# Performance work log

Hardware: AMD Instinct MI355X
Metric: run time of the kernel (lower is better)

Reference implementation:

```python
import jax, jax.numpy as jnp
import numpy as np
import math

SR = 24000
NH = 100      # num_harmonics
NF = 5        # num_formants
HID = 128
TWO_PI = 2.0 * math.pi


def conv1d(x, w, b, groups=1):
    # x: [B,C,T], w: [O, C//groups, K] (torch OIH layout), 'same' padding
    pad = (w.shape[-1] - 1) // 2
    y = jax.lax.conv_general_dilated(
        x, w, window_strides=(1,), padding=[(pad, pad)],
        dimension_numbers=('NCH', 'OIH', 'NCH'), feature_group_count=groups)
    return y + b[None, :, None]


def lrelu(x):
    return jnp.where(x >= 0, x, 0.1 * x)


def interp_linear(x, L):
    # torch F.interpolate(mode='linear', align_corners=False): x [B,C,T] -> [B,C,L]
    B, C, T = x.shape
    pos = (jnp.arange(L, dtype=x.dtype) + 0.5) * (T / L) - 0.5
    pos = jnp.clip(pos, 0.0, float(T - 1))
    lo = jnp.floor(pos).astype(jnp.int32)
    hi = jnp.minimum(lo + 1, T - 1)
    w = pos - lo.astype(x.dtype)
    return x[:, :, lo] * (1.0 - w) + x[:, :, hi] * w


def setup_inputs():
    key = jax.random.key(0)
    ks = jax.random.split(key, 30)
    ki = iter(range(30))
    def p(shape, s=0.05):
        return s * jax.random.normal(ks[next(ki)], shape, jnp.float32)
    B, T, L = 4, 500, 120000
    inp = {}
    # f0 in [80,120) Hz so actual_harmonics == num_harmonics (static shapes, see notes)
    inp['f0'] = 80.0 + 40.0 * jax.random.uniform(ks[next(ki)], (B, T), jnp.float32)
    inp['condition'] = jax.random.normal(ks[next(ki)], (B, HID, T), jnp.float32)
    # harmonic_amplitude_net params
    inp['ha_w1'] = p((HID, 1, 3));   inp['ha_b1'] = p((HID,))
    inp['ha_w2'] = p((256, HID, 1)); inp['ha_b2'] = p((256,))
    inp['ha_w3'] = p((256, 1, 3));   inp['ha_b3'] = p((256,))
    inp['ha_w4'] = p((256, 256, 1)); inp['ha_b4'] = p((256,))
    inp['ha_w5'] = p((NH, 256, 1));  inp['ha_b5'] = p((NH,))
    # formant predictor params
    inp['fm_w1'] = p((256, HID, 3));    inp['fm_b1'] = p((256,))
    inp['fm_w2'] = p((256, 256, 3));    inp['fm_b2'] = p((256,))
    inp['fm_w3'] = p((2 * NF, 256, 1)); inp['fm_b3'] = p((2 * NF,))
    # voice quality predictor params
    inp['vq_w1'] = p((128, HID, 3)); inp['vq_b1'] = p((128,))
    inp['vq_w2'] = p((64, 128, 3));  inp['vq_b2'] = p((64,))
    inp['vq_w3'] = p((3, 64, 1));    inp['vq_b3'] = p((3,))
    inp['audio_length'] = L
    return inp


def reference(f0, condition,
              ha_w1, ha_b1, ha_w2, ha_b2, ha_w3, ha_b3, ha_w4, ha_b4, ha_w5, ha_b5,
              fm_w1, fm_b1, fm_w2, fm_b2, fm_w3, fm_b3,
              vq_w1, vq_b1, vq_w2, vq_b2, vq_w3, vq_b3,
              audio_length):
    B, T = f0.shape
    L = audio_length
    # ---- harmonic_amplitude_net: (dw3 -> pw1 -> lrelu) x2 -> pw1 -> softplus ----
    a = lrelu(conv1d(conv1d(condition, ha_w1, ha_b1, groups=HID), ha_w2, ha_b2))
    a = lrelu(conv1d(conv1d(a, ha_w3, ha_b3, groups=256), ha_w4, ha_b4))
    harmonic_amplitudes = jax.nn.softplus(conv1d(a, ha_w5, ha_b5))  # [B,NH,T]
    # ---- FormantNetwork ----
    fp = conv1d(lrelu(conv1d(lrelu(conv1d(condition, fm_w1, fm_b1)), fm_w2, fm_b2)), fm_w3, fm_b3)
    ff = 200.0 + 3300.0 * jax.nn.sigmoid(fp[:, :NF])        # [B,NF,T]
    fbw = 50.0 + 150.0 * jax.nn.softplus(fp[:, NF:])        # [B,NF,T]
    hidx = jnp.arange(1, NH + 1, dtype=f0.dtype)
    hfreq = hidx[None, :, None] * f0[:, None, :]            # [B,NH,T]
    num = fbw ** 2                                          # [B,NF,T]
    den = (hfreq[:, None] - ff[:, :, None]) ** 2 + num[:, :, None]  # [B,NF,NH,T]
    res = num[:, :, None] / jnp.maximum(den, 1e-5)
    gain = jnp.prod(0.8 + 0.2 * res, axis=1)                # [B,NH,T]
    shaped = harmonic_amplitudes * gain
    # ---- VoiceQualityNetwork ----
    q = jax.nn.sigmoid(conv1d(lrelu(conv1d(lrelu(conv1d(condition, vq_w1, vq_b1)), vq_w2, vq_b2)), vq_w3, vq_b3))
    q_up = interp_linear(q, L)                              # [B,3,L]
    jitter = q_up[:, 0] * 0.05
    shimmer = q_up[:, 1] * 0.15
    breath = q_up[:, 2] * 0.3
    # ---- phase integration + harmonic bank ----
    f0_up = interp_linear(f0[:, None, :], L)[:, 0]          # [B,L]
    phase = jnp.cumsum(TWO_PI * f0_up / SR, axis=1)
    nk1, nk2, nk3 = jax.random.split(jax.random.key(42), 3)
    jphase = phase + jitter * jax.random.normal(nk1, phase.shape, phase.dtype)
    mask = (hidx[None, :, None] * f0_up[:, None, :] < SR / 2).astype(f0.dtype)  # [B,NH,L]
    amps_up = interp_linear(shaped, L)                      # [B,NH,L]
    sig = jnp.sum(amps_up * jnp.sin(jphase[:, None, :] * hidx[None, :, None]) * mask, axis=1)
    # ---- voice qualities: shimmer envelope + breath noise ----
    shim_env = 1.0 + jax.random.normal(nk2, sig.shape, sig.dtype) * shimmer
    out = sig * shim_env + jax.random.normal(nk3, sig.shape, sig.dtype) * breath
    return out
```

## Files before the change

kernel.cpp:

```cpp
#include <hip/hip_runtime.h>
#include <stdint.h>

#define B_ 4
#define T_ 500
#define L_ 120000
#define NH_ 100
#define N1_ 7500
#define N2_ 469
#define N2P_ 7504
#define N3_ 30
#define N3P_ 480
#define N4_ 2
#define N4P_ 32

#define ACT_NONE 0
#define ACT_LRELU 1
#define ACT_SOFTPLUS 2
#define ACT_SIGMOID 3

#define CH3 32
#define XN 4352
#define WN 1536
#define BUFA (XN + WN)

typedef const __attribute__((address_space(1))) void* gp1_t;
typedef __attribute__((address_space(3))) void* lp3_t;

__host__ __device__ __forceinline__ uint32_t tf_rotl(uint32_t v, int d) {
  return (v << d) | (v >> (32 - d));
}
__host__ __device__ __forceinline__ void tf_block(uint32_t k0, uint32_t k1,
                                                  uint32_t& x0, uint32_t& x1) {
  uint32_t k2 = k0 ^ k1 ^ 0x1BD11BDAu;
  x0 += k0; x1 += k1;
#define TF_R(d) x0 += x1; x1 = tf_rotl(x1, (d)); x1 ^= x0;
  TF_R(13) TF_R(15) TF_R(26) TF_R(6)   x0 += k1; x1 += k2 + 1u;
  TF_R(17) TF_R(29) TF_R(16) TF_R(24)  x0 += k2; x1 += k0 + 2u;
  TF_R(13) TF_R(15) TF_R(26) TF_R(6)   x0 += k0; x1 += k1 + 3u;
  TF_R(17) TF_R(29) TF_R(16) TF_R(24)  x0 += k1; x1 += k2 + 4u;
  TF_R(13) TF_R(15) TF_R(26) TF_R(6)   x0 += k2; x1 += k0 + 5u;
#undef TF_R
}

__device__ __forceinline__ float erfinv_xla(float x) {
  float w = -log1pf(-(x * x));
  float p;
  if (w < 5.0f) {
    w = w - 2.5f;
    p = 2.81022636e-08f;
    p = fmaf(p, w, 3.43273939e-07f);
    p = fmaf(p, w, -3.5233877e-06f);
    p = fmaf(p, w, -4.39150654e-06f);
    p = fmaf(p, w, 0.00021858087f);
    p = fmaf(p, w, -0.00125372503f);
    p = fmaf(p, w, -0.00417768164f);
    p = fmaf(p, w, 0.246640727f);
    p = fmaf(p, w, 1.50140941f);
  } else {
    w = sqrtf(w) - 3.0f;
    p = -0.000200214257f;
    p = fmaf(p, w, 0.000100950558f);
    p = fmaf(p, w, 0.00134934322f);
    p = fmaf(p, w, -0.00367342844f);
    p = fmaf(p, w, 0.00573950773f);
    p = fmaf(p, w, -0.0076224613f);
    p = fmaf(p, w, 0.00943887047f);
    p = fmaf(p, w, 1.00167406f);
    p = fmaf(p, w, 2.83297682f);
  }
  return p * x;
}

__device__ __forceinline__ float jax_normal(uint32_t k0, uint32_t k1, uint32_t e) {
  uint32_t x0 = 0u, x1 = e;
  tf_block(k0, k1, x0, x1);
  uint32_t bits = x0 ^ x1;
  float u = __uint_as_float((bits >> 9) | 0x3f800000u) - 1.0f;
  float v = __fadd_rn(__fmul_rn(u, 2.0f), -0x1.fffffep-1f);
  v = fmaxf(v, -0x1.fffffep-1f);
  return __fmul_rn((float)1.4142135623730951, erfinv_xla(v));
}

__device__ __forceinline__ float sin_acc(float xf) {
  double x = (double)xf;
  double kd = rint(x * 6.3661977236758138e-01);
  double r = fma(-kd, 1.5707963267948966e+00, x);
  r = fma(-kd, 6.1232339957367660e-17, r);
  float rf = (float)r;
  float y = rf * rf;
  float ps = fmaf(y, 2.7557319e-06f, -1.9841270e-04f);
  ps = fmaf(y, ps, 8.3333335e-03f);
  ps = fmaf(y, ps, -0.16666667f);
  float s = fmaf(rf * y, ps, rf);
  float pc = fmaf(y, -2.7557319e-07f, 2.4801587e-05f);
  pc = fmaf(y, pc, -1.3888889e-03f);
  pc = fmaf(y, pc, 4.1666668e-02f);
  pc = fmaf(y, pc, -0.5f);
  float c = fmaf(y, pc, 1.0f);
  int q = ((int)kd) & 3;
  float rs = (q & 1) ? c : s;
  return (q & 2) ? -rs : rs;
}

__device__ __forceinline__ float apply_act(float v, int act) {
  switch (act) {
    case ACT_LRELU:    return v >= 0.0f ? v : 0.1f * v;
    case ACT_SOFTPLUS: return fmaxf(v, 0.0f) + log1pf(expf(-fabsf(v)));
    case ACT_SIGMOID:  return 1.0f / (1.0f + expf(-v));
  }
  return v;
}


__device__ __forceinline__ void conv3_async(
    const float* __restrict__ x, const float* __restrict__ w,
    const float* __restrict__ bias, float* __restrict__ y,
    const float* __restrict__ zbuf,
    int Cin, int Cout, int o0, int act, int b, int t0, float* smem) {
  int tid = threadIdx.x;
  int lane = tid & 63, og = tid >> 6;
  int tl = 2 * lane;
  int t = t0 + tl;
  int obase = o0 + og * 4;
  float acc[4][2];
#pragma unroll
  for (int i = 0; i < 4; ++i) {
    float bv = (obase + i < Cout) ? bias[obase + i] : 0.0f;
    acc[i][0] = bv; acc[i][1] = bv;
  }
  const int nch = Cin / CH3;
  auto issue = [&](int c, float* buf) {
    int cb = c * CH3;
#pragma unroll
    for (int k = 0; k < 17; ++k) {
      int idx = tid + 256 * k;
      const float* src = zbuf;
      if (idx < CH3 * 130) {
        int cc = idx / 130, j = idx - cc * 130;
        int tt = t0 - 1 + j;
        if (tt >= 0 && tt < T_) src = x + ((size_t)b * Cin + cb + cc) * T_ + tt;
      }
      __builtin_amdgcn_global_load_lds((gp1_t)src, (lp3_t)(buf + idx), 4, 0, 0);
    }
#pragma unroll
    for (int k = 0; k < 6; ++k) {
      int p = tid + 256 * k;
      int cc = p / 48, r = p - cc * 48;
      int oo = r / 3, kk = r - oo * 3;
      const float* src = (o0 + oo < Cout)
          ? w + ((size_t)(o0 + oo) * Cin + cb + cc) * 3 + kk : zbuf;
      __builtin_amdgcn_global_load_lds((gp1_t)src, (lp3_t)(buf + XN + p), 4, 0, 0);
    }
  };
  issue(0, smem);
  for (int c = 0; c < nch; ++c) {
    const float* cur = smem + (c & 1) * BUFA;
    if (c + 1 < nch) {
      issue(c + 1, smem + ((c + 1) & 1) * BUFA);
      asm volatile("s_waitcnt vmcnt(23)" ::: "memory");
    } else {
      asm volatile("s_waitcnt vmcnt(0)" ::: "memory");
    }
    __builtin_amdgcn_s_barrier();
    __builtin_amdgcn_sched_barrier(0);
    const float* sxf = cur;
    const float* swf = cur + XN;
    for (int cc = 0; cc < CH3; ++cc) {
      const float* row = sxf + cc * 130 + tl;
      float2 xa = *(const float2*)row;
      float2 xb = *(const float2*)(row + 2);
      const float4* wq = (const float4*)(swf + cc * 48 + og * 12);
      float4 W0 = wq[0], W1 = wq[1], W2 = wq[2];
      float wl[12] = {W0.x, W0.y, W0.z, W0.w, W1.x, W1.y, W1.z, W1.w,
                      W2.x, W2.y, W2.z, W2.w};
#pragma unroll
      for (int i = 0; i < 4; ++i) {
        float w0 = wl[3 * i], w1 = wl[3 * i + 1], w2 = wl[3 * i + 2];
        acc[i][0] = fmaf(xa.x, w0, acc[i][0]);
        acc[i][0] = fmaf(xa.y, w1, acc[i][0]);
        acc[i][0] = fmaf(xb.x, w2, acc[i][0]);
        acc[i][1] = fmaf(xa.y, w0, acc[i][1]);
        acc[i][1] = fmaf(xb.x, w1, acc[i][1]);
        acc[i][1] = fmaf(xb.y, w2, acc[i][1]);
      }
    }
    __builtin_amdgcn_sched_barrier(0);
    __builtin_amdgcn_s_barrier();
  }
#pragma unroll
  for (int i = 0; i < 4; ++i) {
    int o = obase + i;
    if (o < Cout) {
      if (t < T_)     y[((size_t)b * Cout + o) * T_ + t]     = apply_act(acc[i][0], act);
      if (t + 1 < T_) y[((size_t)b * Cout + o) * T_ + t + 1] = apply_act(acc[i][1], act);
    }
  }
}

__device__ __forceinline__ void dwpw_async(
    const float* __restrict__ x, const float* __restrict__ wd,
    const float* __restrict__ bd, const float* __restrict__ wp,
    const float* __restrict__ bp, float* __restrict__ y,
    const float* __restrict__ zbuf,
    int Cin, int Cout, int o0, int act, int b, int t0, float* smem) {
  int tid = threadIdx.x;
  int lane = tid & 63, og = tid >> 6;
  int tl = 2 * lane;
  int t = t0 + tl;
  int obase = o0 + og * 4;
  float acc[4][2];
#pragma unroll
  for (int i = 0; i < 4; ++i) {
    float bv = (obase + i < Cout) ? bp[obase + i] : 0.0f;
    acc[i][0] = bv; acc[i][1] = bv;
  }
  const int nch = Cin / CH3;
  auto issue = [&](int c, float* buf) {
    int cb = c * CH3;
#pragma unroll
    for (int k = 0; k < 17; ++k) {
      int idx = tid + 256 * k;
      const float* src = zbuf;
      if (idx < CH3 * 130) {
        int cc = idx / 130, j = idx - cc * 130;
        int tt = t0 - 1 + j;
        if (tt >= 0 && tt < T_) src = x + ((size_t)b * Cin + cb + cc) * T_ + tt;
      }
      __builtin_amdgcn_global_load_lds((gp1_t)src, (lp3_t)(buf + idx), 4, 0, 0);
    }
#pragma unroll
    for (int k = 0; k < 3; ++k) {
      int p = tid + 256 * k;
      const float* src = zbuf;
      if (p < 128) {
        int cc = p >> 2, q = p & 3;
        src = (q < 3) ? wd + (size_t)(cb + cc) * 3 + q : bd + cb + cc;
      } else if (p < 640) {
        int pp = p - 128;
        int cc = pp >> 4, oo = pp & 15;
        if (o0 + oo < Cout) src = wp + (size_t)(o0 + oo) * Cin + cb + cc;
      }
      __builtin_amdgcn_global_load_lds((gp1_t)src, (lp3_t)(buf + XN + p), 4, 0, 0);
    }
  };
  issue(0, smem);
  for (int c = 0; c < nch; ++c) {
    const float* cur = smem + (c & 1) * BUFA;
    if (c + 1 < nch) {
      issue(c + 1, smem + ((c + 1) & 1) * BUFA);
      asm volatile("s_waitcnt vmcnt(20)" ::: "memory");
    } else {
      asm volatile("s_waitcnt vmcnt(0)" ::: "memory");
    }
    __builtin_amdgcn_s_barrier();
    __builtin_amdgcn_sched_barrier(0);
    const float* sxf  = cur;
    const float* swdf = cur + XN;
    const float* swpf = cur + XN + 128;
    for (int cc = 0; cc < CH3; ++cc) {
      const float* row = sxf + cc * 130 + tl;
      float2 xa = *(const float2*)row;
      float2 xb = *(const float2*)(row + 2);
      float4 D = *(const float4*)(swdf + cc * 4);
      float d0 = fmaf(xa.x, D.x, fmaf(xa.y, D.y, fmaf(xb.x, D.z, D.w)));
      float d1 = fmaf(xa.y, D.x, fmaf(xb.x, D.y, fmaf(xb.y, D.z, D.w)));
      float4 Wp = *(const float4*)(swpf + cc * 16 + og * 4);
      acc[0][0] = fmaf(d0, Wp.x, acc[0][0]);
      acc[1][0] = fmaf(d0, Wp.y, acc[1][0]);
      acc[2][0] = fmaf(d0, Wp.z, acc[2][0]);
      acc[3][0] = fmaf(d0, Wp.w, acc[3][0]);
      acc[0][1] = fmaf(d1, Wp.x, acc[0][1]);
      acc[1][1] = fmaf(d1, Wp.y, acc[1][1]);
      acc[2][1] = fmaf(d1, Wp.z, acc[2][1]);
      acc[3][1] = fmaf(d1, Wp.w, acc[3][1]);
    }
    __builtin_amdgcn_sched_barrier(0);
    __builtin_amdgcn_s_barrier();
  }
#pragma unroll
  for (int i = 0; i < 4; ++i) {
    int o = obase + i;
    if (o < Cout) {
      if (t < T_)     y[((size_t)b * Cout + o) * T_ + t]     = apply_act(acc[i][0], act);
      if (t + 1 < T_) y[((size_t)b * Cout + o) * T_ + t + 1] = apply_act(acc[i][1], act);
    }
  }
}

__device__ __forceinline__ void pw_stream(
    const float* __restrict__ x, const float* __restrict__ w,
    const float* __restrict__ bias, float* __restrict__ y,
    int Cin, int Cout, int o0, int act, int b, int t0, float* smem) {
  for (int idx = threadIdx.x; idx < 16 * Cin; idx += 256) {
    int oo = idx / Cin, cc = idx - oo * Cin;
    smem[cc * 16 + oo] = (o0 + oo < Cout) ? w[(size_t)(o0 + oo) * Cin + cc] : 0.0f;
  }
  __syncthreads();
  int lane = threadIdx.x & 63, og = threadIdx.x >> 6;
  int t = t0 + lane;
  int obase = o0 + og * 4;
  float acc[4];
#pragma unroll
  for (int i = 0; i < 4; ++i)
    acc[i] = (obase + i < Cout) ? bias[obase + i] : 0.0f;
  if (t < T_) {
    const float* xr = x + (size_t)b * Cin * T_ + t;
#pragma unroll 4
    for (int cc = 0; cc < Cin; ++cc) {
      float xv = xr[(size_t)cc * T_];
      float4 Wp = *(const float4*)(smem + cc * 16 + og * 4);
      acc[0] = fmaf(xv, Wp.x, acc[0]);
      acc[1] = fmaf(xv, Wp.y, acc[1]);
      acc[2] = fmaf(xv, Wp.z, acc[2]);
      acc[3] = fmaf(xv, Wp.w, acc[3]);
    }
#pragma unroll
    for (int i = 0; i < 4; ++i) {
      int o = obase + i;
      if (o < Cout) y[((size_t)b * Cout + o) * T_ + t] = apply_act(acc[i], act);
    }
  }
}

__device__ void terms_body(const float* __restrict__ f0, float* __restrict__ A1,
                           int base, int stride) {
  const float RINV = (float)(500.0 / 120000.0);
  for (int gid = base; gid < B_ * N1_; gid += stride) {
    int b = gid / N1_, w = gid - b * N1_;
    const float* f0b = f0 + (size_t)b * T_;
    float* a = A1 + (size_t)b * L_ + (size_t)w * 16;
    float S = 0.0f;
    int lbase = w * 16;
    for (int i = 0; i < 16; ++i) {
      int l = lbase + i;
      float pos = __fsub_rn(__fmul_rn(__fadd_rn((float)l, 0.5f), RINV), 0.5f);
      pos = fminf(fmaxf(pos, 0.0f), 499.0f);
      int lo = (int)floorf(pos);
      int hi = lo + 1; hi = hi < (T_ - 1) ? hi : (T_ - 1);
      float wt = __fsub_rn(pos, (float)lo);
      float omw = __fsub_rn(1.0f, wt);
      float f0up = __fadd_rn(__fmul_rn(f0b[lo], omw), __fmul_rn(f0b[hi], wt));
      float trm = __fdiv_rn(__fmul_rn((float)6.283185307179586, f0up), 24000.0f);
      S = __fadd_rn(S, trm);
      a[i] = S;
    }
  }
}

__device__ void rwr_body(const float* __restrict__ A1, float* __restrict__ A2,
                         float* __restrict__ A3, float* __restrict__ A4,
                         float* __restrict__ E5, float* __restrict__ E3o,
                         float* __restrict__ E2o) {
  int tid = threadIdx.x;
  for (int gid = tid; gid < B_ * N2_; gid += 256) {
    int b = gid / N2_, w = gid - b * N2_;
    float S = 0.0f;
    for (int m = 0; m < 16; ++m) {
      int i = w * 16 + m;
      float v = (i < N1_) ? A1[(size_t)b * L_ + (size_t)i * 16 + 15] : 0.0f;
      S = __fadd_rn(S, v);
      A2[(size_t)b * N2P_ + i] = S;
    }
  }
  __syncthreads();
  for (int gid = tid; gid < B_ * N3_; gid += 256) {
    int b = gid / N3_, w = gid - b * N3_;
    float S = 0.0f;
    for (int m = 0; m < 16; ++m) {
      int i = w * 16 + m;
      float v = (i < N2_) ? A2[(size_t)b * N2P_ + (size_t)i * 16 + 15] : 0.0f;
      S = __fadd_rn(S, v);
      A3[(size_t)b * N3P_ + i] = S;
    }
  }
  __syncthreads();
  for (int gid = tid; gid < B_ * N4_; gid += 256) {
    int b = gid / N4_, w = gid - b * N4_;
    float S = 0.0f;
    for (int m = 0; m < 16; ++m) {
      int i = w * 16 + m;
      float v = (i < N3_) ? A3[(size_t)b * N3P_ + (size_t)i * 16 + 15] : 0.0f;
      S = __fadd_rn(S, v);
      A4[(size_t)b * N4P_ + i] = S;
    }
  }
  __syncthreads();
  if (tid < B_) {
    E5[tid * N4_ + 0] = 0.0f;
    E5[tid * N4_ + 1] = A4[(size_t)tid * N4P_ + 15];
  }
  __syncthreads();
  for (int gid = tid; gid < B_ * N3_; gid += 256) {
    int b = gid / N3_, k = gid - b * N3_;
    float v = 0.0f;
    if (k > 0) {
      int i = k - 1;
      v = __fadd_rn(E5[b * N4_ + (i >> 4)], A4[(size_t)b * N4P_ + i]);
    }
    E3o[b * N3_ + k] = v;
  }
  __syncthreads();
  for (int gid = tid; gid < B_ * N2_; gid += 256) {
    int b = gid / N2_, j = gid - b * N2_;
    float v = 0.0f;
    if (j > 0) {
      int i = j - 1;
      v = __fadd_rn(E3o[b * N3_ + (i >> 4)], A3[(size_t)b * N3P_ + i]);
    }
    E2o[b * N2_ + j] = v;
  }
}

__global__ void __launch_bounds__(256) conv_l1(
    const float* __restrict__ cond, const float* __restrict__ f0,
    const float* __restrict__ fw1, const float* __restrict__ fb1,
    const float* __restrict__ vw1, const float* __restrict__ vb1,
    const float* __restrict__ hw1, const float* __restrict__ hb1,
    const float* __restrict__ hw2, const float* __restrict__ hb2,
    float* __restrict__ fmA, float* __restrict__ vqB, float* __restrict__ haB,
    float* __restrict__ A1, const float* __restrict__ zbuf) {
  __shared__ __align__(16) float smem[2 * BUFA];
  int yy = blockIdx.y, b = blockIdx.z, t0 = blockIdx.x * 128;
  if (yy < 16) {
    conv3_async(cond, fw1, fb1, fmA, zbuf, 128, 256, yy * 16, ACT_LRELU, b, t0, smem);
  } else if (yy < 24) {
    conv3_async(cond, vw1, vb1, vqB, zbuf, 128, 128, (yy - 16) * 16, ACT_LRELU, b, t0, smem);
  } else if (yy < 40) {
    dwpw_async(cond, hw1, hb1, hw2, hb2, haB, zbuf, 128, 256, (yy - 24) * 16, ACT_LRELU, b, t0, smem);
  } else {
    int base = (blockIdx.z * 4 + blockIdx.x) * 256 + threadIdx.x;
    terms_body(f0, A1, base, 4096);
  }
}

__global__ void __launch_bounds__(256) conv_l2(
    const float* __restrict__ fmA, const float* __restrict__ vqB,
    const float* __restrict__ haB,
    const float* __restrict__ fw2, const float* __restrict__ fb2,
    const float* __restrict__ vw2, const float* __restrict__ vb2,
    const float* __restrict__ hw3, const float* __restrict__ hb3,
    const float* __restrict__ hw4, const float* __restrict__ hb4,
    float* __restrict__ fmC, float* __restrict__ vqC, float* __restrict__ haC,
    const float* __restrict__ A1, float* __restrict__ A2, float* __restrict__ A3,
    float* __restrict__ A4, float* __restrict__ E5, float* __restrict__ E3o,
    float* __restrict__ E2o, const float* __restrict__ zbuf) {
  __shared__ __align__(16) float smem[2 * BUFA];
  int yy = blockIdx.y, b = blockIdx.z, t0 = blockIdx.x * 128;
  if (yy < 16) {
    conv3_async(fmA, fw2, fb2, fmC, zbuf, 256, 256, yy * 16, ACT_LRELU, b, t0, smem);
  } else if (yy < 20) {
    conv3_async(vqB, vw2, vb2, vqC, zbuf, 128, 64, (yy - 16) * 16, ACT_LRELU, b, t0, smem);
  } else if (yy < 36) {
    dwpw_async(haB, hw3, hb3, hw4, hb4, haC, zbuf, 256, 256, (yy - 20) * 16, ACT_LRELU, b, t0, smem);
  } else {
    if (blockIdx.x != 0 || blockIdx.z != 0) return;
    rwr_body(A1, A2, A3, A4, E5, E3o, E2o);
  }
}

__global__ void __launch_bounds__(256) conv_l3(
    const float* __restrict__ haC, const float* __restrict__ fmC,
    const float* __restrict__ vqC,
    const float* __restrict__ hw5, const float* __restrict__ hb5,
    const float* __restrict__ fw3, const float* __restrict__ fb3,
    const float* __restrict__ vw3, const float* __restrict__ vb3,
    float* __restrict__ ha, float* __restrict__ fp, float* __restrict__ qv) {
  __shared__ __align__(16) float smem[4096];
  int yy = blockIdx.y, b = blockIdx.z, t0 = blockIdx.x * 64;
  if (yy < 7) {
    pw_stream(haC, hw5, hb5, ha, 256, 100, yy * 16, ACT_SOFTPLUS, b, t0, smem);
  } else if (yy == 7) {
    pw_stream(fmC, fw3, fb3, fp, 256, 10, 0, ACT_NONE, b, t0, smem);
  } else {
    pw_stream(vqC, vw3, vb3, qv, 64, 3, 0, ACT_SIGMOID, b, t0, smem);
  }
}

__global__ void __launch_bounds__(256) main_kernel(
    const float* __restrict__ A1, const float* __restrict__ A2,
    const float* __restrict__ E2o,
    const float* __restrict__ ha, const float* __restrict__ fp,
    const float* __restrict__ q,
    const float* __restrict__ f0, float* __restrict__ out,
    uint32_t k10, uint32_t k11, uint32_t k20, uint32_t k21, uint32_t k30, uint32_t k31) {
  const float RINV = (float)(500.0 / 120000.0);
  int b = blockIdx.y;
  int l0 = blockIdx.x * 256;
  int l = l0 + threadIdx.x;
  __shared__ float ls[4][NH_];
  __shared__ float sff[4][5], snm[4][5];
  float p0 = __fsub_rn(__fmul_rn(__fadd_rn((float)l0, 0.5f), RINV), 0.5f);
  p0 = fminf(fmaxf(p0, 0.0f), 499.0f);
  int lo0 = (int)floorf(p0);
  if (threadIdx.x < 40) {
    int j = threadIdx.x / 10, h = threadIdx.x - j * 10;
    int col = lo0 + j; col = col < (T_ - 1) ? col : (T_ - 1);
    float v = fp[((size_t)b * 10 + h) * T_ + col];
    if (h < 5) {
      sff[j][h] = 200.0f + 3300.0f * (1.0f / (1.0f + expf(-v)));
    } else {
      float bw = 50.0f + 150.0f * (fmaxf(v, 0.0f) + log1pf(expf(-fabsf(v))));
      snm[j][h - 5] = bw * bw;
    }
  }
  __syncthreads();
  for (int i = threadIdx.x; i < 4 * NH_; i += 256) {
    int j = i / NH_, h = i - j * NH_;
    int col = lo0 + j; col = col < (T_ - 1) ? col : (T_ - 1);
    float hfreq = (float)(h + 1) * f0[(size_t)b * T_ + col];
    float g = 1.0f;
    for (int ii = 0; ii < 5; ++ii) {
      float d = hfreq - sff[j][ii];
      float den = d * d + snm[j][ii];
      float res = snm[j][ii] / fmaxf(den, 1e-5f);
      g = g * (0.8f + 0.2f * res);
    }
    ls[j][h] = ha[((size_t)b * NH_ + h) * T_ + col] * g;
  }
  __syncthreads();
  if (l >= L_) return;

  float pos = __fsub_rn(__fmul_rn(__fadd_rn((float)l, 0.5f), RINV), 0.5f);
  pos = fminf(fmaxf(pos, 0.0f), 499.0f);
  int lo = (int)floorf(pos);
  int hi = lo + 1; hi = hi < (T_ - 1) ? hi : (T_ - 1);
  float w = __fsub_rn(pos, (float)lo);
  float omw = __fsub_rn(1.0f, w);

  const float* f0b = f0 + (size_t)b * T_;
  float f0up = __fadd_rn(__fmul_rn(f0b[lo], omw), __fmul_rn(f0b[hi], w));
  const float* qb = q + (size_t)b * 3 * T_;
  float q0 = __fadd_rn(__fmul_rn(qb[lo], omw), __fmul_rn(qb[hi], w));
  float q1 = __fadd_rn(__fmul_rn(qb[T_ + lo], omw), __fmul_rn(qb[T_ + hi], w));
  float q2 = __fadd_rn(__fmul_rn(qb[2 * T_ + lo], omw), __fmul_rn(qb[2 * T_ + hi], w));
  float jit = __fmul_rn(q0, 0.05f);
  float shm = __fmul_rn(q1, 0.15f);
  float brt = __fmul_rn(q2, 0.3f);

  uint32_t e = (uint32_t)(b * L_ + l);
  float n1 = jax_normal(k10, k11, e);
  float n2 = jax_normal(k20, k21, e);
  float n3 = jax_normal(k30, k31, e);

  float e1v = 0.0f;
  int r = l >> 4;
  if (r > 0) {
    int i = r - 1;
    e1v = __fadd_rn(E2o[b * N2_ + (i >> 4)], A2[(size_t)b * N2P_ + i]);
  }
  float phf = __fadd_rn(e1v, A1[(size_t)b * L_ + l]);
  float jph = __fadd_rn(phf, __fmul_rn(jit, n1));

  int jlo = lo - lo0;
  int jhi = hi - lo0; jhi = jhi < 3 ? jhi : 3;

  float acc = 0.0f;
  for (int h = 1; h <= NH_; ++h) {
    float amp = __fadd_rn(__fmul_rn(ls[jlo][h - 1], omw), __fmul_rn(ls[jhi][h - 1], w));
    float hf = (float)h;
    float arg = __fmul_rn(jph, hf);
    float s = sin_acc(arg);
    float m = (__fmul_rn(hf, f0up) < 12000.0f) ? 1.0f : 0.0f;
    acc = __fadd_rn(acc, __fmul_rn(__fmul_rn(amp, s), m));
  }
  float env = __fadd_rn(1.0f, __fmul_rn(n2, shm));
  out[(size_t)b * L_ + l] = __fadd_rn(__fmul_rn(acc, env), __fmul_rn(n3, brt));
}

extern "C" void kernel_launch(void* const* d_in, const int* in_sizes, int n_in,
                              void* d_out, int out_size, void* d_ws, size_t ws_size,
                              hipStream_t stream) {
  const float* f0    = (const float*)d_in[0];
  const float* cond  = (const float*)d_in[1];
  const float* ha_w1 = (const float*)d_in[2];
  const float* ha_b1 = (const float*)d_in[3];
  const float* ha_w2 = (const float*)d_in[4];
  const float* ha_b2 = (const float*)d_in[5];
  const float* ha_w3 = (const float*)d_in[6];
  const float* ha_b3 = (const float*)d_in[7];
  const float* ha_w4 = (const float*)d_in[8];
  const float* ha_b4 = (const float*)d_in[9];
  const float* ha_w5 = (const float*)d_in[10];
  const float* ha_b5 = (const float*)d_in[11];
  const float* fm_w1 = (const float*)d_in[12];
  const float* fm_b1 = (const float*)d_in[13];
  const float* fm_w2 = (const float*)d_in[14];
  const float* fm_b2 = (const float*)d_in[15];
  const float* fm_w3 = (const float*)d_in[16];
  const float* fm_b3 = (const float*)d_in[17];
  const float* vq_w1 = (const float*)d_in[18];
  const float* vq_b1 = (const float*)d_in[19];
  const float* vq_w2 = (const float*)d_in[20];
  const float* vq_b2 = (const float*)d_in[21];
  const float* vq_w3 = (const float*)d_in[22];
  const float* vq_b3 = (const float*)d_in[23];
  float* out = (float*)d_out;

  uint32_t kw[3][2];
  for (uint32_t j = 0; j < 3; ++j) {
    uint32_t x0 = 0u, x1 = j;
    tf_block(0u, 42u, x0, x1);
    kw[j][0] = x0; kw[j][1] = x1;
  }

  float* ws = (float*)d_ws;
  size_t off = 0;
  auto take = [&](size_t n) { float* p = ws + off; off += (n + 3) & ~(size_t)3; return p; };
  float* fmA = take(512000);
  float* haB = take(512000);
  float* fmC = take(512000);
  float* haC = take(512000);
  float* vqB = take(256000);
  float* vqC = take(128000);
  float* A1  = take((size_t)B_ * L_);
  float* A2  = take((size_t)B_ * N2P_);
  float* A3  = take((size_t)B_ * N3P_);
  float* A4  = take((size_t)B_ * N4P_);
  float* E5  = take((size_t)B_ * N4_);
  float* E3o = take((size_t)B_ * N3_);
  float* E2o = take((size_t)B_ * N2_);
  float* zbuf = take(64);
  float* ha = fmA;
  float* fp = vqB;
  float* qv = vqB + 20480;

  hipMemsetAsync(zbuf, 0, 64 * sizeof(float), stream);

  conv_l1<<<dim3(4, 41, B_), 256, 0, stream>>>(
      cond, f0, fm_w1, fm_b1, vq_w1, vq_b1, ha_w1, ha_b1, ha_w2, ha_b2,
      fmA, vqB, haB, A1, zbuf);
  conv_l2<<<dim3(4, 37, B_), 256, 0, stream>>>(
      fmA, vqB, haB, fm_w2, fm_b2, vq_w2, vq_b2, ha_w3, ha_b3, ha_w4, ha_b4,
      fmC, vqC, haC, A1, A2, A3, A4, E5, E3o, E2o, zbuf);
  conv_l3<<<dim3(8, 9, B_), 256, 0, stream>>>(
      haC, fmC, vqC, ha_w5, ha_b5, fm_w3, fm_b3, vq_w3, vq_b3, ha, fp, qv);
  main_kernel<<<dim3((L_ + 255) / 256, B_), 256, 0, stream>>>(
      A1, A2, E2o, ha, fp, qv, f0, out,
      kw[0][0], kw[0][1], kw[1][0], kw[1][1], kw[2][0], kw[2][1]);
  (void)in_sizes; (void)n_in; (void)out_size; (void)ws_size;
}
```

Baseline: 281.5 us.

## Widen conv time tiles to four outputs per thread and halve channel chunk

The conv3 and depthwise-pointwise conv kernels now compute 4 time steps per thread instead of 2, covering 256 time steps per block, and stage 16 input channels per chunk instead of 32. The number of blocks in the time dimension for conv_l1 and conv_l2 halves, and the terms work is re-partitioned to match. Each thread gets more register reuse of weights and inputs, and outputs are written with vectorized float4 stores. The cost is fewer blocks (less parallelism on a large GPU) and more pipeline iterations per block.

```diff
diff --git a/kernel.cpp b/kernel.cpp
--- a/kernel.cpp
+++ b/kernel.cpp
@@ -18,9 +18,10 @@
 #define ACT_SOFTPLUS 2
 #define ACT_SIGMOID 3
 
-#define CH3 32
+#define CH 16
+#define ROWS 260
 #define XN 4352
-#define WN 1536
+#define WN 768
 #define BUFA (XN + WN)
 
 typedef const __attribute__((address_space(1))) void* gp1_t;
@@ -119,127 +120,35 @@
     int Cin, int Cout, int o0, int act, int b, int t0, float* smem) {
   int tid = threadIdx.x;
   int lane = tid & 63, og = tid >> 6;
-  int tl = 2 * lane;
+  int tl = 4 * lane;
   int t = t0 + tl;
   int obase = o0 + og * 4;
-  float acc[4][2];
+  float acc[4][4];
 #pragma unroll
   for (int i = 0; i < 4; ++i) {
     float bv = (obase + i < Cout) ? bias[obase + i] : 0.0f;
-    acc[i][0] = bv; acc[i][1] = bv;
-  }
-  const int nch = Cin / CH3;
+#pragma unroll
+    for (int j = 0; j < 4; ++j) acc[i][j] = bv;
+  }
+  const int nch = Cin / CH;
   auto issue = [&](int c, float* buf) {
-    int cb = c * CH3;
+    int cb = c * CH;
 #pragma unroll
     for (int k = 0; k < 17; ++k) {
       int idx = tid + 256 * k;
-      const float* src = zbuf;
-      if (idx < CH3 * 130) {
-        int cc = idx / 130, j = idx - cc * 130;
-        int tt = t0 - 1 + j;
-        if (tt >= 0 && tt < T_) src = x + ((size_t)b * Cin + cb + cc) * T_ + tt;
-      }
+      int cc = idx / ROWS, j = idx - cc * ROWS;
+      int tt = t0 - 1 + j;
+      const float* src = (cc < CH && j < 258 && tt >= 0 && tt < T_)
+          ? x + ((size_t)b * Cin + cb + cc) * T_ + tt : zbuf;
       __builtin_amdgcn_global_load_lds((gp1_t)src, (lp3_t)(buf + idx), 4, 0, 0);
     }
 #pragma unroll
-    for (int k = 0; k < 6; ++k) {
+    for (int k = 0; k < 3; ++k) {
       int p = tid + 256 * k;
       int cc = p / 48, r = p - cc * 48;
       int oo = r / 3, kk = r - oo * 3;
       const float* src = (o0 + oo < Cout)
           ? w + ((size_t)(o0 + oo) * Cin + cb + cc) * 3 + kk : zbuf;
-      __builtin_amdgcn_global_load_lds((gp1_t)src, (lp3_t)(buf + XN + p), 4, 0, 0);
-    }
-  };
-  issue(0, smem);
-  for (int c = 0; c < nch; ++c) {
-    const float* cur = smem + (c & 1) * BUFA;
-    if (c + 1 < nch) {
-      issue(c + 1, smem + ((c + 1) & 1) * BUFA);
-      asm volatile("s_waitcnt vmcnt(23)" ::: "memory");
-    } else {
-      asm volatile("s_waitcnt vmcnt(0)" ::: "memory");
-    }
-    __builtin_amdgcn_s_barrier();
-    __builtin_amdgcn_sched_barrier(0);
-    const float* sxf = cur;
-    const float* swf = cur + XN;
-    for (int cc = 0; cc < CH3; ++cc) {
-      const float* row = sxf + cc * 130 + tl;
-      float2 xa = *(const float2*)row;
-      float2 xb = *(const float2*)(row + 2);
-      const float4* wq = (const float4*)(swf + cc * 48 + og * 12);
-      float4 W0 = wq[0], W1 = wq[1], W2 = wq[2];
-      float wl[12] = {W0.x, W0.y, W0.z, W0.w, W1.x, W1.y, W1.z, W1.w,
-                      W2.x, W2.y, W2.z, W2.w};
-#pragma unroll
-      for (int i = 0; i < 4; ++i) {
-        float w0 = wl[3 * i], w1 = wl[3 * i + 1], w2 = wl[3 * i + 2];
-        acc[i][0] = fmaf(xa.x, w0, acc[i][0]);
-        acc[i][0] = fmaf(xa.y, w1, acc[i][0]);
-        acc[i][0] = fmaf(xb.x, w2, acc[i][0]);
-        acc[i][1] = fmaf(xa.y, w0, acc[i][1]);
-        acc[i][1] = fmaf(xb.x, w1, acc[i][1]);
-        acc[i][1] = fmaf(xb.y, w2, acc[i][1]);
-      }
-    }
-    __builtin_amdgcn_sched_barrier(0);
-    __builtin_amdgcn_s_barrier();
-  }
-#pragma unroll
-  for (int i = 0; i < 4; ++i) {
-    int o = obase + i;
-    if (o < Cout) {
-      if (t < T_)     y[((size_t)b * Cout + o) * T_ + t]     = apply_act(acc[i][0], act);
-      if (t + 1 < T_) y[((size_t)b * Cout + o) * T_ + t + 1] = apply_act(acc[i][1], act);
-    }
-  }
-}
-
-__device__ __forceinline__ void dwpw_async(
-    const float* __restrict__ x, const float* __restrict__ wd,
-    const float* __restrict__ bd, const float* __restrict__ wp,
-    const float* __restrict__ bp, float* __restrict__ y,
-    const float* __restrict__ zbuf,
-    int Cin, int Cout, int o0, int act, int b, int t0, float* smem) {
-  int tid = threadIdx.x;
-  int lane = tid & 63, og = tid >> 6;
-  int tl = 2 * lane;
-  int t = t0 + tl;
-  int obase = o0 + og * 4;
-  float acc[4][2];
-#pragma unroll
-  for (int i = 0; i < 4; ++i) {
-    float bv = (obase + i < Cout) ? bp[obase + i] : 0.0f;
-    acc[i][0] = bv; acc[i][1] = bv;
-  }
-  const int nch = Cin / CH3;
-  auto issue = [&](int c, float* buf) {
-    int cb = c * CH3;
-#pragma unroll
-    for (int k = 0; k < 17; ++k) {
-      int idx = tid + 256 * k;
-      const float* src = zbuf;
-      if (idx < CH3 * 130) {
-        int cc = idx / 130, j = idx - cc * 130;
-        int tt = t0 - 1 + j;
-        if (tt >= 0 && tt < T_) src = x + ((size_t)b * Cin + cb + cc) * T_ + tt;
-      }
-      __builtin_amdgcn_global_load_lds((gp1_t)src, (lp3_t)(buf + idx), 4, 0, 0);
-    }
-#pragma unroll
-    for (int k = 0; k < 3; ++k) {
-      int p = tid + 256 * k;
-      const float* src = zbuf;
-      if (p < 128) {
-        int cc = p >> 2, q = p & 3;
-        src = (q < 3) ? wd + (size_t)(cb + cc) * 3 + q : bd + cb + cc;
-      } else if (p < 640) {
-        int pp = p - 128;
-        int cc = pp >> 4, oo = pp & 15;
-        if (o0 + oo < Cout) src = wp + (size_t)(o0 + oo) * Cin + cb + cc;
-      }
       __builtin_amdgcn_global_load_lds((gp1_t)src, (lp3_t)(buf + XN + p), 4, 0, 0);
     }
   };
@@ -254,25 +163,27 @@
     }
     __builtin_amdgcn_s_barrier();
     __builtin_amdgcn_sched_barrier(0);
-    const float* sxf  = cur;
-    const float* swdf = cur + XN;
-    const float* swpf = cur + XN + 128;
-    for (int cc = 0; cc < CH3; ++cc) {
-      const float* row = sxf + cc * 130 + tl;
-      float2 xa = *(const float2*)row;
-      float2 xb = *(const float2*)(row + 2);
-      float4 D = *(const float4*)(swdf + cc * 4);
-      float d0 = fmaf(xa.x, D.x, fmaf(xa.y, D.y, fmaf(xb.x, D.z, D.w)));
-      float d1 = fmaf(xa.y, D.x, fmaf(xb.x, D.y, fmaf(xb.y, D.z, D.w)));
-      float4 Wp = *(const float4*)(swpf + cc * 16 + og * 4);
-      acc[0][0] = fmaf(d0, Wp.x, acc[0][0]);
-      acc[1][0] = fmaf(d0, Wp.y, acc[1][0]);
-      acc[2][0] = fmaf(d0, Wp.z, acc[2][0]);
-      acc[3][0] = fmaf(d0, Wp.w, acc[3][0]);
-      acc[0][1] = fmaf(d1, Wp.x, acc[0][1]);
-      acc[1][1] = fmaf(d1, Wp.y, acc[1][1]);
-      acc[2][1] = fmaf(d1, Wp.z, acc[2][1]);
-      acc[3][1] = fmaf(d1, Wp.w, acc[3][1]);
+    const float* sxf = cur;
+    const float* swf = cur + XN;
+    for (int cc = 0; cc < CH; ++cc) {
+      const float* row = sxf + cc * ROWS + tl;
+      float4 X0 = *(const float4*)row;
+      float2 X1 = *(const float2*)(row + 4);
+      float xw[6] = {X0.x, X0.y, X0.z, X0.w, X1.x, X1.y};
+      const float4* wq = (const float4*)(swf + cc * 48 + og * 12);
+      float4 W0 = wq[0], W1 = wq[1], W2 = wq[2];
+      float wl[12] = {W0.x, W0.y, W0.z, W0.w, W1.x, W1.y, W1.z, W1.w,
+                      W2.x, W2.y, W2.z, W2.w};
+#pragma unroll
+      for (int i = 0; i < 4; ++i) {
+        float w0 = wl[3 * i], w1 = wl[3 * i + 1], w2 = wl[3 * i + 2];
+#pragma unroll
+        for (int j = 0; j < 4; ++j) {
+          acc[i][j] = fmaf(xw[j],     w0, acc[i][j]);
+          acc[i][j] = fmaf(xw[j + 1], w1, acc[i][j]);
+          acc[i][j] = fmaf(xw[j + 2], w2, acc[i][j]);
+        }
+      }
     }
     __builtin_amdgcn_sched_barrier(0);
     __builtin_amdgcn_s_barrier();
@@ -281,8 +192,112 @@
   for (int i = 0; i < 4; ++i) {
     int o = obase + i;
     if (o < Cout) {
-      if (t < T_)     y[((size_t)b * Cout + o) * T_ + t]     = apply_act(acc[i][0], act);
-      if (t + 1 < T_) y[((size_t)b * Cout + o) * T_ + t + 1] = apply_act(acc[i][1], act);
+      float* yp = y + ((size_t)b * Cout + o) * T_ + t;
+      if (t + 4 <= T_) {
+        *(float4*)yp = make_float4(apply_act(acc[i][0], act), apply_act(acc[i][1], act),
+                                   apply_act(acc[i][2], act), apply_act(acc[i][3], act));
+      } else {
+#pragma unroll
+        for (int j = 0; j < 4; ++j)
+          if (t + j < T_) yp[j] = apply_act(acc[i][j], act);
+      }
+    }
+  }
+}
+
+__device__ __forceinline__ void dwpw_async(
+    const float* __restrict__ x, const float* __restrict__ wd,
+    const float* __restrict__ bd, const float* __restrict__ wp,
+    const float* __restrict__ bp, float* __restrict__ y,
+    const float* __restrict__ zbuf,
+    int Cin, int Cout, int o0, int act, int b, int t0, float* smem) {
+  int tid = threadIdx.x;
+  int lane = tid & 63, og = tid >> 6;
+  int tl = 4 * lane;
+  int t = t0 + tl;
+  int obase = o0 + og * 4;
+  float acc[4][4];
+#pragma unroll
+  for (int i = 0; i < 4; ++i) {
+    float bv = (obase + i < Cout) ? bp[obase + i] : 0.0f;
+#pragma unroll
+    for (int j = 0; j < 4; ++j) acc[i][j] = bv;
+  }
+  const int nch = Cin / CH;
+  auto issue = [&](int c, float* buf) {
+    int cb = c * CH;
+#pragma unroll
+    for (int k = 0; k < 17; ++k) {
+      int idx = tid + 256 * k;
+      int cc = idx / ROWS, j = idx - cc * ROWS;
+      int tt = t0 - 1 + j;
+      const float* src = (cc < CH && j < 258 && tt >= 0 && tt < T_)
+          ? x + ((size_t)b * Cin + cb + cc) * T_ + tt : zbuf;
+      __builtin_amdgcn_global_load_lds((gp1_t)src, (lp3_t)(buf + idx), 4, 0, 0);
+    }
+#pragma unroll
+    for (int k = 0; k < 2; ++k) {
+      int p = tid + 256 * k;
+      const float* src = zbuf;
+      if (p < 64) {
+        int cc = p >> 2, q = p & 3;
+        src = (q < 3) ? wd + (size_t)(cb + cc) * 3 + q : bd + cb + cc;
+      } else if (p < 320) {
+        int pp = p - 64;
+        int cc = pp >> 4, oo = pp & 15;
+        if (o0 + oo < Cout) src = wp + (size_t)(o0 + oo) * Cin + cb + cc;
+      }
+      __builtin_amdgcn_global_load_lds((gp1_t)src, (lp3_t)(buf + XN + p), 4, 0, 0);
+    }
+  };
+  issue(0, smem);
+  for (int c = 0; c < nch; ++c) {
+    const float* cur = smem + (c & 1) * BUFA;
+    if (c + 1 < nch) {
+      issue(c + 1, smem + ((c + 1) & 1) * BUFA);
+      asm volatile("s_waitcnt vmcnt(19)" ::: "memory");
+    } else {
+      asm volatile("s_waitcnt vmcnt(0)" ::: "memory");
+    }
+    __builtin_amdgcn_s_barrier();
+    __builtin_amdgcn_sched_barrier(0);
+    const float* sxf  = cur;
+    const float* swdf = cur + XN;
+    const float* swpf = cur + XN + 64;
+    for (int cc = 0; cc < CH; ++cc) {
+      const float* row = sxf + cc * ROWS + tl;
+      float4 X0 = *(const float4*)row;
+      float2 X1 = *(const float2*)(row + 4);
+      float xw[6] = {X0.x, X0.y, X0.z, X0.w, X1.x, X1.y};
+      float4 D = *(const float4*)(swdf + cc * 4);
+      float d[4];
+#pragma unroll
+      for (int j = 0; j < 4; ++j)
+        d[j] = fmaf(xw[j], D.x, fmaf(xw[j + 1], D.y, fmaf(xw[j + 2], D.z, D.w)));
+      float4 Wp = *(const float4*)(swpf + cc * 16 + og * 4);
+      float wl[4] = {Wp.x, Wp.y, Wp.z, Wp.w};
+#pragma unroll
+      for (int i = 0; i < 4; ++i)
+#pragma unroll
+        for (int j = 0; j < 4; ++j)
+          acc[i][j] = fmaf(d[j], wl[i], acc[i][j]);
+    }
+    __builtin_amdgcn_sched_barrier(0);
+    __builtin_amdgcn_s_barrier();
+  }
+#pragma unroll
+  for (int i = 0; i < 4; ++i) {
+    int o = obase + i;
+    if (o < Cout) {
+      float* yp = y + ((size_t)b * Cout + o) * T_ + t;
+      if (t + 4 <= T_) {
+        *(float4*)yp = make_float4(apply_act(acc[i][0], act), apply_act(acc[i][1], act),
+                                   apply_act(acc[i][2], act), apply_act(acc[i][3], act));
+      } else {
+#pragma unroll
+        for (int j = 0; j < 4; ++j)
+          if (t + j < T_) yp[j] = apply_act(acc[i][j], act);
+      }
     }
   }
 }
@@ -420,7 +435,7 @@
     float* __restrict__ fmA, float* __restrict__ vqB, float* __restrict__ haB,
     float* __restrict__ A1, const float* __restrict__ zbuf) {
   __shared__ __align__(16) float smem[2 * BUFA];
-  int yy = blockIdx.y, b = blockIdx.z, t0 = blockIdx.x * 128;
+  int yy = blockIdx.y, b = blockIdx.z, t0 = blockIdx.x * 256;
   if (yy < 16) {
     conv3_async(cond, fw1, fb1, fmA, zbuf, 128, 256, yy * 16, ACT_LRELU, b, t0, smem);
   } else if (yy < 24) {
@@ -428,8 +443,8 @@
   } else if (yy < 40) {
     dwpw_async(cond, hw1, hb1, hw2, hb2, haB, zbuf, 128, 256, (yy - 24) * 16, ACT_LRELU, b, t0, smem);
   } else {
-    int base = (blockIdx.z * 4 + blockIdx.x) * 256 + threadIdx.x;
-    terms_body(f0, A1, base, 4096);
+    int base = (blockIdx.z * 2 + blockIdx.x) * 256 + threadIdx.x;
+    terms_body(f0, A1, base, 2048);
   }
 }
 
@@ -445,7 +460,7 @@
     float* __restrict__ A4, float* __restrict__ E5, float* __restrict__ E3o,
     float* __restrict__ E2o, const float* __restrict__ zbuf) {
   __shared__ __align__(16) float smem[2 * BUFA];
-  int yy = blockIdx.y, b = blockIdx.z, t0 = blockIdx.x * 128;
+  int yy = blockIdx.y, b = blockIdx.z, t0 = blockIdx.x * 256;
   if (yy < 16) {
     conv3_async(fmA, fw2, fb2, fmC, zbuf, 256, 256, yy * 16, ACT_LRELU, b, t0, smem);
   } else if (yy < 20) {
@@ -626,10 +641,10 @@
 
   hipMemsetAsync(zbuf, 0, 64 * sizeof(float), stream);
 
-  conv_l1<<<dim3(4, 41, B_), 256, 0, stream>>>(
+  conv_l1<<<dim3(2, 41, B_), 256, 0, stream>>>(
       cond, f0, fm_w1, fm_b1, vq_w1, vq_b1, ha_w1, ha_b1, ha_w2, ha_b2,
       fmA, vqB, haB, A1, zbuf);
-  conv_l2<<<dim3(4, 37, B_), 256, 0, stream>>>(
+  conv_l2<<<dim3(2, 37, B_), 256, 0, stream>>>(
       fmA, vqB, haB, fm_w2, fm_b2, vq_w2, vq_b2, ha_w3, ha_b3, ha_w4, ha_b4,
       fmC, vqC, haC, A1, A2, A3, A4, E5, E3o, E2o, zbuf);
   conv_l3<<<dim3(8, 9, B_), 256, 0, stream>>>(
```

Result: slower. 316.1 us (+12.3%).
